# Kernel optimization log

Hardware: AMD Instinct MI355X
Metric: run time of the kernel (lower is better)

Reference implementation:

```python
import jax, jax.numpy as jnp
import numpy as np
from jax import lax

B, N, D_PTS = 8, 4096, 6
N_POINTS, N_SAMPLES, RADIUS = 1024, 32, 0.2
MLPS = [64, 64, 128]
BN_EPS = 1e-3  # keras BatchNormalization default epsilon


def safe_norm(diff, axis):
    # euclidean norm with a backward-safe sqrt (same forward values)
    sq = jnp.sum(diff * diff, axis=axis)
    pos = sq > 0
    return jnp.where(pos, jnp.sqrt(jnp.where(pos, sq, 1.0)), 0.0)


def setup_inputs() -> dict:
    key = jax.random.key(0)
    ks = jax.random.split(key, 2)
    xyz = jax.random.normal(ks[0], (B, N, 3), jnp.float32)
    points = jax.random.normal(ks[1], (B, N, D_PTS), jnp.float32)
    inp = {"xyz": xyz, "points": points}
    c_in = 3 + D_PTS
    for i, c_out in enumerate(MLPS):
        kw = jax.random.fold_in(key, 100 + i)
        inp[f"w{i}"] = jax.random.normal(kw, (c_in, c_out), jnp.float32) * (1.0 / np.sqrt(c_in))
        inp[f"b{i}"] = jnp.zeros((c_out,), jnp.float32)
        inp[f"g{i}"] = jnp.ones((c_out,), jnp.float32)
        inp[f"be{i}"] = jnp.zeros((c_out,), jnp.float32)
        c_in = c_out
    return inp


def fps(xyz, n_points):
    # farthest point sampling; original seeds with a random index, we use 0 deterministically
    b, n, _ = xyz.shape
    init_idx = jnp.zeros((b,), jnp.int32)
    mask0 = jnp.ones((b, n), xyz.dtype)
    def step(carry, _):
        mask, last = carry
        added = jnp.take_along_axis(xyz, last[:, None, None], axis=1)  # [B,1,D]
        dist = safe_norm(xyz - added, 2) * mask                        # [B,N]
        nxt = jnp.argmax(dist, axis=1).astype(jnp.int32)
        new_mask = jnp.minimum(dist * mask * 1e11, mask)
        return (new_mask, nxt), nxt
    _, ids = lax.scan(step, (mask0, init_idx), None, length=n_points - 1)
    return jnp.concatenate([init_idx[:, None], ids.T], axis=1)  # [B, n_points]


def gather_points(x, idx):
    # x: [B,N,C]; idx: [B,...] -> [B,...,C]
    b = x.shape[0]
    flat = idx.reshape(b, -1)
    out = jnp.take_along_axis(x, flat[..., None], axis=1)
    return out.reshape(idx.shape + (x.shape[-1],))


def query_ball(radius, n_samples, xyz, cent_xyz):
    # faithful to source: compares norm to radius**2 (source quirk), full argsort then slice
    diff = xyz[:, None, :, :] - cent_xyz[:, :, None, :]   # [B,n,N,3]
    dist = safe_norm(diff, 3)                              # [B,n,N]
    dist = jnp.minimum(dist, radius * radius)
    return jnp.argsort(dist, axis=2)[:, :, :n_samples]     # [B,n,n_samples]


def mlp_layer(h, w, b, g, be):
    # pointwise Dense + BatchNormalization (batch stats, axis=-1) + relu
    h = jnp.einsum('bnsc,cd->bnsd', h, w) + b
    mean = jnp.mean(h, axis=(0, 1, 2), keepdims=True)
    var = jnp.var(h, axis=(0, 1, 2), keepdims=True)
    h = g * (h - mean) * lax.rsqrt(var + BN_EPS) + be
    return jax.nn.relu(h)


def forward(xyz, points, params):
    cent_idx = fps(xyz, N_POINTS)                 # [B, n_points]
    cent_xyz = gather_points(xyz, cent_idx)       # [B, n_points, 3]
    group_idx = query_ball(RADIUS, N_SAMPLES, xyz, cent_xyz)  # [B, n_points, n_samples]
    group_xyz = gather_points(xyz, group_idx)     # [B, n_points, n_samples, 3]
    group_pts = gather_points(points, group_idx)  # [B, n_points, n_samples, D]
    h = jnp.concatenate([group_xyz, group_pts], axis=-1)
    for (w, b, g, be) in params:
        h = mlp_layer(h, w, b, g, be)
    return cent_xyz, jnp.max(h, axis=2)           # [B,n_points,3], [B,n_points,128]


def reference(xyz, points, w0, b0, g0, be0, w1, b1, g1, be1, w2, b2, g2, be2):
    params = [(w0, b0, g0, be0), (w1, b1, g1, be1), (w2, b2, g2, be2)]
    return forward(xyz, points, params)
```

## Files before the change

kernel.cpp:

```cpp
#include <hip/hip_runtime.h>

#define NPTS  4096
#define NB    8
#define NC    1024
#define NSAMP 32
#define DP    6
#define C0    9
#define C3    128
#define ROWS_TOT 262144

#define OFF_SS   (32ull<<10)
#define OFF_Y0   (16ull<<20)
#define OFF_Y1   (96ull<<20)
#define OFF_PSUM (168ull<<20)
#define OFF_PSQ  (172ull<<20)
#define OFF_GMX  (176ull<<20)
#define OFF_GMN  (180ull<<20)

typedef unsigned long long ull;

__device__ __forceinline__ float sqdist_noc(float x, float y, float z,
                                            float cx, float cy, float cz) {
  #pragma clang fp contract(off)
  float dx = x - cx, dy = y - cy, dz = z - cz;
  return dx * dx + dy * dy + dz * dz;
}

template <int CTRL, int RM>
__device__ __forceinline__ float dpp_mov_f(float x) {
  int xi = __float_as_int(x);
  int r = __builtin_amdgcn_update_dpp(xi, xi, CTRL, RM, 0xf, false);
  return __int_as_float(r);
}

__device__ __forceinline__ float wave64_fmax(float x) {
  x = fmaxf(x, dpp_mov_f<0x111, 0xf>(x));
  x = fmaxf(x, dpp_mov_f<0x112, 0xf>(x));
  x = fmaxf(x, dpp_mov_f<0x114, 0xf>(x));
  x = fmaxf(x, dpp_mov_f<0x118, 0xf>(x));
  x = fmaxf(x, dpp_mov_f<0x142, 0xa>(x));
  x = fmaxf(x, dpp_mov_f<0x143, 0xc>(x));
  return x;
}

__global__ __launch_bounds__(256)
void fps_kernel(const float* __restrict__ xyz, float* __restrict__ cent) {
  const int b = blockIdx.x;
  const int t = threadIdx.x;
  const float* X = xyz + (size_t)b * NPTS * 3;
  float* OC = cent + (size_t)b * NC * 3;

  __shared__ float4 sxyz[NPTS];
  __shared__ float4 wkc[2][4];
  __shared__ alignas(16) int wki[2][4];
  __shared__ int sidx[NC];

  for (int p = t; p < NPTS; p += 256)
    sxyz[p] = make_float4(X[p * 3 + 0], X[p * 3 + 1], X[p * 3 + 2], 0.f);
  __syncthreads();

  float px[16], py[16], pz[16], h[16];
  #pragma unroll
  for (int i = 0; i < 16; i++) {
    float4 v = sxyz[t * 16 + i];
    px[i] = v.x; py[i] = v.y; pz[i] = v.z;
    h[i] = fmaf(v.x, v.x, fmaf(v.y, v.y, v.z * v.z));
  }

  const int wv = t >> 6;
  float4 c;

  auto step_body = [&](int pw_) {
    const float c2x = c.x + c.x, c2y = c.y + c.y, c2z = c.z + c.z;
    float key[16]; int idx[16];
    #pragma unroll
    for (int i = 0; i < 16; i++) {
      key[i] = fmaf(pz[i], -c2z, fmaf(py[i], -c2y, fmaf(px[i], -c2x, h[i])));
      idx[i] = i;
    }
    #pragma unroll
    for (int s = 1; s < 16; s <<= 1) {
      #pragma unroll
      for (int i = 0; i < 16; i += 2 * s) {
        bool tk = key[i + s] > key[i];
        key[i] = tk ? key[i + s] : key[i];
        idx[i] = tk ? idx[i + s] : idx[i];
      }
    }
    const float mx = key[0];
    const int mj = idx[0];
    float4 cand = sxyz[(t << 4) + mj];
    float wm = wave64_fmax(mx);
    float smax = __int_as_float(__builtin_amdgcn_readlane(__float_as_int(wm), 63));
    if (mx == smax) {
      wkc[pw_][wv] = make_float4(cand.x, cand.y, cand.z, smax);
      wki[pw_][wv] = (t << 4) + mj;
    }
  };

  auto fold = [&](int pr_) -> int {
    float4 q0 = wkc[pr_][0], q1 = wkc[pr_][1];
    float4 q2 = wkc[pr_][2], q3 = wkc[pr_][3];
    const int4 ii = *(const int4*)&wki[pr_][0];
    bool g1 = q1.w > q0.w; float4 ca = g1 ? q1 : q0; int ia = g1 ? ii.y : ii.x;
    bool g3 = q3.w > q2.w; float4 cb = g3 ? q3 : q2; int ib = g3 ? ii.w : ii.z;
    bool gb = cb.w > ca.w; c = gb ? cb : ca; return gb ? ib : ia;
  };

  if (t == 0) { sidx[0] = 0; h[0] = -__builtin_inff(); }
  c = sxyz[0];
  step_body(1);
  __syncthreads();

  for (int k = 2; k < NC; k++) {
    const int pr = (k - 1) & 1, pw = k & 1;
    int gidx = fold(pr);
    if (t == 0) sidx[k - 1] = gidx;
    if ((gidx >> 4) == t) {
      int m = gidx & 15;
      #pragma unroll
      for (int i = 0; i < 16; i++)
        if (i == m) h[i] = -__builtin_inff();
    }
    step_body(pw);
    __syncthreads();
  }
  {
    int gidx = fold(1023 & 1);
    if (t == 0) sidx[NC - 1] = gidx;
  }
  __syncthreads();
  for (int i = t; i < NC; i += 256) {
    float4 cc = sxyz[sidx[i]];
    OC[i * 3 + 0] = cc.x;
    OC[i * 3 + 1] = cc.y;
    OC[i * 3 + 2] = cc.z;
  }
}

#define BCAP 256
__global__ __launch_bounds__(256)
void ball_dense0_kernel(const float* __restrict__ xyz, const float* __restrict__ pts,
                        const float* __restrict__ cent,
                        const float* __restrict__ W0, const float* __restrict__ b0,
                        float* __restrict__ y0,
                        float* __restrict__ psum, float* __restrict__ psq) {
  const int blk = blockIdx.x;
  const int b = blk >> 10;
  const int t = threadIdx.x;
  const float* X = xyz + (size_t)b * NPTS * 3;
  const float* P = pts + (size_t)b * NPTS * DP;
  const float cx = cent[(size_t)blk * 3 + 0];
  const float cy = cent[(size_t)blk * 3 + 1];
  const float cz = cent[(size_t)blk * 3 + 2];

  __shared__ int scount;
  __shared__ ull skeys[BCAP];
  __shared__ ull ssorted[BCAP];
  __shared__ int sel[NSAMP];
  __shared__ float xs0[NSAMP * C0];
  __shared__ float w0s[C0 * 64];
  __shared__ float b0s[64];
  __shared__ float red[2][NSAMP][64];
  if (t == 0) scount = 0;
  for (int e = t; e < C0 * 64; e += 256) w0s[e] = W0[e];
  if (t < 64) b0s[t] = b0[t];
  __syncthreads();

  #pragma unroll
  for (int i = 0; i < 16; i++) {
    int j = t * 16 + i;
    float sq = sqdist_noc(X[j * 3 + 0], X[j * 3 + 1], X[j * 3 + 2], cx, cy, cz);
    if (sq < 0.0017f) {
      float d = (sq > 0.f) ? sqrtf(sq) : 0.f;
      if (d < 0.04f) {
        int pos = atomicAdd(&scount, 1);
        if (pos < BCAP)
          skeys[pos] = ((ull)(unsigned)__float_as_int(d) << 12) | (unsigned)j;
      }
    }
  }
  __syncthreads();
  const int M = min(scount, BCAP);

  if (t < M) {
    ull my = skeys[t];
    int r = 0;
    for (int j2 = 0; j2 < M; j2++) r += (skeys[j2] < my);
    ssorted[r] = my;
  }
  __syncthreads();

  if (t < NSAMP) {
    int v;
    if (t < M) {
      v = (int)(ssorted[t] & 0xFFFull);
    } else {
      int s = t - M;
      int idx = s;
      for (int it = 0; it < 40; it++) {
        int c = 0;
        for (int j2 = 0; j2 < M; j2++) c += ((int)(skeys[j2] & 0xFFFull) <= idx);
        int nidx = s + c;
        if (nidx == idx) break;
        idx = nidx;
      }
      v = idx;
    }
    sel[t] = v;
  }
  __syncthreads();

  for (int e = t; e < NSAMP * C0; e += 256) {
    int k = e / C0;
    int cc = e - k * C0;
    int j = sel[k];
    xs0[e] = (cc < 3) ? X[j * 3 + cc] : P[j * DP + (cc - 3)];
  }
  __syncthreads();

  const int row = t >> 3, c8 = (t & 7) * 8;
  float a[8];
  #pragma unroll
  for (int j = 0; j < 8; j++) a[j] = b0s[c8 + j];
  #pragma unroll
  for (int k = 0; k < C0; k++) {
    float xv = xs0[row * C0 + k];
    #pragma unroll
    for (int j = 0; j < 8; j++) a[j] = fmaf(xv, w0s[k * 64 + c8 + j], a[j]);
  }
  float* Y = y0 + ((size_t)blk * NSAMP + row) * 64 + c8;
  *(float4*)(Y + 0) = make_float4(a[0], a[1], a[2], a[3]);
  *(float4*)(Y + 4) = make_float4(a[4], a[5], a[6], a[7]);
  #pragma unroll
  for (int j = 0; j < 8; j++) red[0][row][c8 + j] = a[j];
  #pragma unroll
  for (int j = 0; j < 8; j++) red[1][row][c8 + j] = a[j] * a[j];
  __syncthreads();
  if (t < 64) {
    float S = 0.f, Q = 0.f;
    #pragma unroll
    for (int g = 0; g < NSAMP; g++) { S += red[0][g][t]; Q += red[1][g][t]; }
    psum[(size_t)t * 8192 + blk] = S;
    psq [(size_t)t * 8192 + blk] = Q;
  }
}

template <int RPB, int COUT, int CGN, int NBLKS, bool MM>
__global__ __launch_bounds__(256)
void dense_mid_kernel(const float* __restrict__ yin, const float* __restrict__ ssin,
                      const float* __restrict__ W, const float* __restrict__ bias,
                      float* __restrict__ yout,
                      float* __restrict__ psum, float* __restrict__ psq,
                      float* __restrict__ gmax, float* __restrict__ gmin) {
  constexpr int NG = 256 / CGN;
  __shared__ float xs[RPB * 68];
  __shared__ float ws[64 * COUT];
  __shared__ float scs[64], shs[64];
  __shared__ float red[2][NG][COUT];
  __shared__ float redm[MM ? 2 : 1][MM ? NG : 1][MM ? COUT : 1];
  const int blk = blockIdx.x, t = threadIdx.x;
  if (t < 64) { scs[t] = ssin[t]; shs[t] = ssin[128 + t]; }
  __syncthreads();
  const size_t rbase = (size_t)blk * RPB;
  for (int e = t; e < RPB * 64; e += 256) {
    int c = e & 63;
    float v = yin[rbase * 64 + e];
    xs[(e >> 6) * 68 + c] = fmaxf(fmaf(v, scs[c], shs[c]), 0.f);
  }
  for (int e = t; e < 64 * COUT; e += 256) ws[e] = W[e];
  __syncthreads();
  const int rg = t / CGN, cg = t % CGN;
  float acc[4][4];
  float4 bv = *(const float4*)(bias + cg * 4);
  #pragma unroll
  for (int r = 0; r < 4; r++) { acc[r][0] = bv.x; acc[r][1] = bv.y; acc[r][2] = bv.z; acc[r][3] = bv.w; }
  for (int k0 = 0; k0 < 64; k0 += 4) {
    float4 xv[4];
    #pragma unroll
    for (int r = 0; r < 4; r++)
      xv[r] = *(const float4*)(xs + (rg * 4 + r) * 68 + k0);
    #pragma unroll
    for (int kk = 0; kk < 4; kk++) {
      float4 wv = *(const float4*)(ws + (k0 + kk) * COUT + cg * 4);
      #pragma unroll
      for (int r = 0; r < 4; r++) {
        float x = (&xv[r].x)[kk];
        acc[r][0] = fmaf(x, wv.x, acc[r][0]);
        acc[r][1] = fmaf(x, wv.y, acc[r][1]);
        acc[r][2] = fmaf(x, wv.z, acc[r][2]);
        acc[r][3] = fmaf(x, wv.w, acc[r][3]);
      }
    }
  }
  if constexpr (!MM) {
    #pragma unroll
    for (int r = 0; r < 4; r++)
      *(float4*)(yout + (rbase + rg * 4 + r) * COUT + cg * 4) =
          make_float4(acc[r][0], acc[r][1], acc[r][2], acc[r][3]);
  }
  #pragma unroll
  for (int c4 = 0; c4 < 4; c4++) {
    float s = 0.f, q = 0.f;
    #pragma unroll
    for (int r = 0; r < 4; r++) { float v = acc[r][c4]; s += v; q = fmaf(v, v, q); }
    red[0][rg][cg * 4 + c4] = s;
    red[1][rg][cg * 4 + c4] = q;
    if constexpr (MM) {
      float mx = acc[0][c4], mn = acc[0][c4];
      #pragma unroll
      for (int r = 1; r < 4; r++) { mx = fmaxf(mx, acc[r][c4]); mn = fminf(mn, acc[r][c4]); }
      redm[0][rg][cg * 4 + c4] = mx;
      redm[1][rg][cg * 4 + c4] = mn;
    }
  }
  __syncthreads();
  if (t < COUT) {
    float S = 0.f, Q = 0.f;
    #pragma unroll
    for (int g = 0; g < NG; g++) { S += red[0][g][t]; Q += red[1][g][t]; }
    psum[(size_t)t * NBLKS + blk] = S;
    psq [(size_t)t * NBLKS + blk] = Q;
    if constexpr (MM) {
      float mx = redm[0][0][t], mn = redm[1][0][t];
      #pragma unroll
      for (int g = 1; g < NG; g++) { mx = fmaxf(mx, redm[0][g][t]); mn = fminf(mn, redm[1][g][t]); }
      gmax[(size_t)blk * COUT + t] = mx;
      gmin[(size_t)blk * COUT + t] = mn;
    }
  }
}

template <int NBLK>
__global__ __launch_bounds__(256)
void stats_final_kernel(const float* __restrict__ psum, const float* __restrict__ psq,
                        const float* __restrict__ g, const float* __restrict__ be,
                        float* __restrict__ ss_out) {
  const int c = blockIdx.x, t = threadIdx.x;
  float S = 0.f, Q = 0.f;
  for (int i = t; i < NBLK; i += 256) {
    S += psum[(size_t)c * NBLK + i];
    Q += psq [(size_t)c * NBLK + i];
  }
  __shared__ float sS[256], sQ[256];
  sS[t] = S; sQ[t] = Q;
  __syncthreads();
  #pragma unroll
  for (int off = 128; off; off >>= 1) {
    if (t < off) { sS[t] += sS[t + off]; sQ[t] += sQ[t + off]; }
    __syncthreads();
  }
  if (t == 0) {
    const float inv = 1.0f / 262144.0f;
    float mean = sS[0] * inv;
    float var = sQ[0] * inv - mean * mean;
    float scale = g[c] / sqrtf(var + 1e-3f);
    ss_out[c] = scale;
    ss_out[128 + c] = be[c] - mean * scale;
  }
}

__global__ __launch_bounds__(128)
void pool_final_kernel(const float* __restrict__ gmax, const float* __restrict__ gmin,
                       const float* __restrict__ ss2, float* __restrict__ out1) {
  const int blk = blockIdx.x, c = threadIdx.x;
  const float sc = ss2[c], sh = ss2[128 + c];
  float v = (sc >= 0.f) ? gmax[(size_t)blk * C3 + c] : gmin[(size_t)blk * C3 + c];
  out1[(size_t)blk * C3 + c] = fmaxf(fmaf(v, sc, sh), 0.f);
}

extern "C" void kernel_launch(void* const* d_in, const int* in_sizes, int n_in,
                              void* d_out, int out_size, void* d_ws, size_t ws_size,
                              hipStream_t stream) {
  const float* xyz = (const float*)d_in[0];
  const float* pts = (const float*)d_in[1];
  const float* w0 = (const float*)d_in[2];
  const float* b0 = (const float*)d_in[3];
  const float* g0 = (const float*)d_in[4];
  const float* be0 = (const float*)d_in[5];
  const float* w1 = (const float*)d_in[6];
  const float* b1 = (const float*)d_in[7];
  const float* g1 = (const float*)d_in[8];
  const float* be1 = (const float*)d_in[9];
  const float* w2 = (const float*)d_in[10];
  const float* b2 = (const float*)d_in[11];
  const float* g2 = (const float*)d_in[12];
  const float* be2 = (const float*)d_in[13];

  float* out = (float*)d_out;
  float* cent = out;
  float* out1 = out + (size_t)NB * NC * 3;

  char* ws = (char*)d_ws;
  float* ssA  = (float*)(ws + OFF_SS);
  float* y0   = (float*)(ws + OFF_Y0);
  float* y1   = (float*)(ws + OFF_Y1);
  float* psum = (float*)(ws + OFF_PSUM);
  float* psq  = (float*)(ws + OFF_PSQ);
  float* gmx  = (float*)(ws + OFF_GMX);
  float* gmn  = (float*)(ws + OFF_GMN);

  fps_kernel<<<dim3(NB), dim3(256), 0, stream>>>(xyz, cent);

  ball_dense0_kernel<<<dim3(NB * NC), dim3(256), 0, stream>>>(
      xyz, pts, cent, w0, b0, y0, psum, psq);
  stats_final_kernel<8192><<<dim3(64), dim3(256), 0, stream>>>(psum, psq, g0, be0, ssA + 0 * 256);

  dense_mid_kernel<64, 64, 16, 4096, false><<<dim3(ROWS_TOT / 64), dim3(256), 0, stream>>>(
      y0, ssA + 0 * 256, w1, b1, y1, psum, psq, nullptr, nullptr);
  stats_final_kernel<4096><<<dim3(64), dim3(256), 0, stream>>>(psum, psq, g1, be1, ssA + 1 * 256);

  dense_mid_kernel<32, 128, 32, 8192, true><<<dim3(ROWS_TOT / 32), dim3(256), 0, stream>>>(
      y1, ssA + 1 * 256, w2, b2, nullptr, psum, psq, gmx, gmn);
  stats_final_kernel<8192><<<dim3(128), dim3(256), 0, stream>>>(psum, psq, g2, be2, ssA + 2 * 256);

  pool_final_kernel<<<dim3(NB * NC), dim3(128), 0, stream>>>(gmx, gmn, ssA + 2 * 256, out1);

  (void)in_sizes; (void)n_in; (void)out_size; (void)ws_size;
}
```

Measured before the change: 880.8 us.

## Use one-row-per-thread dense kernels with uniform weight reads and transposed reductions

The shared-memory tiled register-blocked dense kernels for layers 1 and 2 are replaced by kernels where each thread computes a full output row. Weights are read straight from global memory with wave-uniform indices, so they can become scalar loads, and the input tile staging through LDS is removed. Per-channel sum, sum of squares and per-centroid max/min are computed by transposing accumulators through padded LDS. Holding 64 accumulators plus 64 inputs per thread raises register pressure and may lower occupancy. The non-coalesced per-thread row loads are another risk.

```diff
diff --git a/kernel.cpp b/kernel.cpp
--- a/kernel.cpp
+++ b/kernel.cpp
@@ -246,88 +246,131 @@
   }
 }
 
-template <int RPB, int COUT, int CGN, int NBLKS, bool MM>
 __global__ __launch_bounds__(256)
-void dense_mid_kernel(const float* __restrict__ yin, const float* __restrict__ ssin,
-                      const float* __restrict__ W, const float* __restrict__ bias,
-                      float* __restrict__ yout,
-                      float* __restrict__ psum, float* __restrict__ psq,
-                      float* __restrict__ gmax, float* __restrict__ gmin) {
-  constexpr int NG = 256 / CGN;
-  __shared__ float xs[RPB * 68];
-  __shared__ float ws[64 * COUT];
-  __shared__ float scs[64], shs[64];
-  __shared__ float red[2][NG][COUT];
-  __shared__ float redm[MM ? 2 : 1][MM ? NG : 1][MM ? COUT : 1];
-  const int blk = blockIdx.x, t = threadIdx.x;
-  if (t < 64) { scs[t] = ssin[t]; shs[t] = ssin[128 + t]; }
-  __syncthreads();
-  const size_t rbase = (size_t)blk * RPB;
-  for (int e = t; e < RPB * 64; e += 256) {
-    int c = e & 63;
-    float v = yin[rbase * 64 + e];
-    xs[(e >> 6) * 68 + c] = fmaxf(fmaf(v, scs[c], shs[c]), 0.f);
-  }
-  for (int e = t; e < 64 * COUT; e += 256) ws[e] = W[e];
-  __syncthreads();
-  const int rg = t / CGN, cg = t % CGN;
-  float acc[4][4];
-  float4 bv = *(const float4*)(bias + cg * 4);
-  #pragma unroll
-  for (int r = 0; r < 4; r++) { acc[r][0] = bv.x; acc[r][1] = bv.y; acc[r][2] = bv.z; acc[r][3] = bv.w; }
+void dense_lane1_kernel(const float* __restrict__ y0, const float* __restrict__ ss0,
+                        const float* __restrict__ W1, const float* __restrict__ b1,
+                        float* __restrict__ y1,
+                        float* __restrict__ psum, float* __restrict__ psq) {
+  __shared__ float tr[4][64][33];
+  __shared__ float wred[2][4][64];
+  const int t = threadIdx.x, wid = t >> 6, lane = t & 63;
+  const size_t row = (size_t)blockIdx.x * 256 + (size_t)(wid * 64 + lane);
+  float acc[64];
+  #pragma unroll
+  for (int c = 0; c < 64; c++) acc[c] = b1[c];
+  const float* Xr = y0 + row * 64;
+  #pragma unroll 1
   for (int k0 = 0; k0 < 64; k0 += 4) {
-    float4 xv[4];
-    #pragma unroll
-    for (int r = 0; r < 4; r++)
-      xv[r] = *(const float4*)(xs + (rg * 4 + r) * 68 + k0);
+    float4 xv = *(const float4*)(Xr + k0);
     #pragma unroll
     for (int kk = 0; kk < 4; kk++) {
-      float4 wv = *(const float4*)(ws + (k0 + kk) * COUT + cg * 4);
+      const int k = k0 + kk;
+      float x = fmaxf(fmaf((&xv.x)[kk], ss0[k], ss0[128 + k]), 0.f);
+      const float* Wk = W1 + k * 64;
       #pragma unroll
-      for (int r = 0; r < 4; r++) {
-        float x = (&xv[r].x)[kk];
-        acc[r][0] = fmaf(x, wv.x, acc[r][0]);
-        acc[r][1] = fmaf(x, wv.y, acc[r][1]);
-        acc[r][2] = fmaf(x, wv.z, acc[r][2]);
-        acc[r][3] = fmaf(x, wv.w, acc[r][3]);
-      }
-    }
-  }
-  if constexpr (!MM) {
-    #pragma unroll
-    for (int r = 0; r < 4; r++)
-      *(float4*)(yout + (rbase + rg * 4 + r) * COUT + cg * 4) =
-          make_float4(acc[r][0], acc[r][1], acc[r][2], acc[r][3]);
-  }
-  #pragma unroll
-  for (int c4 = 0; c4 < 4; c4++) {
-    float s = 0.f, q = 0.f;
-    #pragma unroll
-    for (int r = 0; r < 4; r++) { float v = acc[r][c4]; s += v; q = fmaf(v, v, q); }
-    red[0][rg][cg * 4 + c4] = s;
-    red[1][rg][cg * 4 + c4] = q;
-    if constexpr (MM) {
-      float mx = acc[0][c4], mn = acc[0][c4];
+      for (int c = 0; c < 64; c++) acc[c] = fmaf(x, Wk[c], acc[c]);
+    }
+  }
+  float* Yr = y1 + row * 64;
+  #pragma unroll
+  for (int c0 = 0; c0 < 64; c0 += 4)
+    *(float4*)(Yr + c0) = make_float4(acc[c0], acc[c0 + 1], acc[c0 + 2], acc[c0 + 3]);
+  const int c = lane & 31;
+  const bool isQ = lane >= 32;
+  #pragma unroll
+  for (int chunk = 0; chunk < 2; chunk++) {
+    __syncthreads();
+    #pragma unroll
+    for (int j = 0; j < 32; j++) tr[wid][lane][j] = acc[chunk * 32 + j];
+    __syncthreads();
+    float A = 0.f;
+    for (int r = 0; r < 64; r++) {
+      float v = tr[wid][r][c];
+      A = fmaf(v, isQ ? v : 1.0f, A);
+    }
+    wred[isQ ? 1 : 0][wid][chunk * 32 + c] = A;
+  }
+  __syncthreads();
+  if (t < 64) {
+    float S = 0.f, Q = 0.f;
+    #pragma unroll
+    for (int w = 0; w < 4; w++) { S += wred[0][w][t]; Q += wred[1][w][t]; }
+    psum[(size_t)t * 1024 + blockIdx.x] = S;
+    psq [(size_t)t * 1024 + blockIdx.x] = Q;
+  }
+}
+
+__global__ __launch_bounds__(256)
+void dense_lane2_kernel(const float* __restrict__ y1, const float* __restrict__ ss1,
+                        const float* __restrict__ W2, const float* __restrict__ b2,
+                        float* __restrict__ psum, float* __restrict__ psq,
+                        float* __restrict__ gmax, float* __restrict__ gmin) {
+  __shared__ float tr[4][64][33];
+  __shared__ float wred[2][4][128];
+  const int t = threadIdx.x, wid = t >> 6, lane = t & 63;
+  const size_t row = (size_t)blockIdx.x * 256 + (size_t)(wid * 64 + lane);
+  const int centA = blockIdx.x * 8 + wid * 2;
+  const int centB = centA + 1;
+
+  float x[64];
+  const float* Xr = y1 + row * 64;
+  #pragma unroll
+  for (int k0 = 0; k0 < 64; k0 += 4) {
+    float4 xv = *(const float4*)(Xr + k0);
+    #pragma unroll
+    for (int kk = 0; kk < 4; kk++)
+      x[k0 + kk] = fmaxf(fmaf((&xv.x)[kk], ss1[k0 + kk], ss1[128 + k0 + kk]), 0.f);
+  }
+
+  const int c = lane & 31;
+  const bool isQ = lane >= 32;
+  #pragma unroll 1
+  for (int half = 0; half < 2; half++) {
+    float acc[64];
+    #pragma unroll
+    for (int cc = 0; cc < 64; cc++) acc[cc] = b2[half * 64 + cc];
+    #pragma unroll 1
+    for (int k = 0; k < 64; k++) {
+      const float* Wk = W2 + k * C3 + half * 64;
+      const float xk = x[k];
       #pragma unroll
-      for (int r = 1; r < 4; r++) { mx = fmaxf(mx, acc[r][c4]); mn = fminf(mn, acc[r][c4]); }
-      redm[0][rg][cg * 4 + c4] = mx;
-      redm[1][rg][cg * 4 + c4] = mn;
-    }
-  }
-  __syncthreads();
-  if (t < COUT) {
+      for (int cc = 0; cc < 64; cc++) acc[cc] = fmaf(xk, Wk[cc], acc[cc]);
+    }
+    #pragma unroll
+    for (int chunk = 0; chunk < 2; chunk++) {
+      __syncthreads();
+      #pragma unroll
+      for (int j = 0; j < 32; j++) tr[wid][lane][j] = acc[chunk * 32 + j];
+      __syncthreads();
+      const int ch = half * 64 + chunk * 32 + c;
+      float A = 0.f, m1 = -__builtin_inff(), m2 = -__builtin_inff();
+      for (int r = 0; r < 32; r++) {
+        float v = tr[wid][r][c];
+        A = fmaf(v, isQ ? v : 1.0f, A);
+        m1 = fmaxf(m1, isQ ? -v : v);
+      }
+      for (int r = 32; r < 64; r++) {
+        float v = tr[wid][r][c];
+        A = fmaf(v, isQ ? v : 1.0f, A);
+        m2 = fmaxf(m2, isQ ? -v : v);
+      }
+      wred[isQ ? 1 : 0][wid][ch] = A;
+      if (!isQ) {
+        gmax[(size_t)centA * C3 + ch] = m1;
+        gmax[(size_t)centB * C3 + ch] = m2;
+      } else {
+        gmin[(size_t)centA * C3 + ch] = -m1;
+        gmin[(size_t)centB * C3 + ch] = -m2;
+      }
+    }
+  }
+  __syncthreads();
+  if (t < C3) {
     float S = 0.f, Q = 0.f;
     #pragma unroll
-    for (int g = 0; g < NG; g++) { S += red[0][g][t]; Q += red[1][g][t]; }
-    psum[(size_t)t * NBLKS + blk] = S;
-    psq [(size_t)t * NBLKS + blk] = Q;
-    if constexpr (MM) {
-      float mx = redm[0][0][t], mn = redm[1][0][t];
-      #pragma unroll
-      for (int g = 1; g < NG; g++) { mx = fmaxf(mx, redm[0][g][t]); mn = fminf(mn, redm[1][g][t]); }
-      gmax[(size_t)blk * COUT + t] = mx;
-      gmin[(size_t)blk * COUT + t] = mn;
-    }
+    for (int w = 0; w < 4; w++) { S += wred[0][w][t]; Q += wred[1][w][t]; }
+    psum[(size_t)t * 1024 + blockIdx.x] = S;
+    psq [(size_t)t * 1024 + blockIdx.x] = Q;
   }
 }
 
@@ -406,13 +449,13 @@
       xyz, pts, cent, w0, b0, y0, psum, psq);
   stats_final_kernel<8192><<<dim3(64), dim3(256), 0, stream>>>(psum, psq, g0, be0, ssA + 0 * 256);
 
-  dense_mid_kernel<64, 64, 16, 4096, false><<<dim3(ROWS_TOT / 64), dim3(256), 0, stream>>>(
-      y0, ssA + 0 * 256, w1, b1, y1, psum, psq, nullptr, nullptr);
-  stats_final_kernel<4096><<<dim3(64), dim3(256), 0, stream>>>(psum, psq, g1, be1, ssA + 1 * 256);
-
-  dense_mid_kernel<32, 128, 32, 8192, true><<<dim3(ROWS_TOT / 32), dim3(256), 0, stream>>>(
-      y1, ssA + 1 * 256, w2, b2, nullptr, psum, psq, gmx, gmn);
-  stats_final_kernel<8192><<<dim3(128), dim3(256), 0, stream>>>(psum, psq, g2, be2, ssA + 2 * 256);
+  dense_lane1_kernel<<<dim3(ROWS_TOT / 256), dim3(256), 0, stream>>>(
+      y0, ssA + 0 * 256, w1, b1, y1, psum, psq);
+  stats_final_kernel<1024><<<dim3(64), dim3(256), 0, stream>>>(psum, psq, g1, be1, ssA + 1 * 256);
+
+  dense_lane2_kernel<<<dim3(ROWS_TOT / 256), dim3(256), 0, stream>>>(
+      y1, ssA + 1 * 256, w2, b2, psum, psq, gmx, gmn);
+  stats_final_kernel<1024><<<dim3(128), dim3(256), 0, stream>>>(psum, psq, g2, be2, ssA + 2 * 256);
 
   pool_final_kernel<<<dim3(NB * NC), dim3(128), 0, stream>>>(gmx, gmn, ssA + 2 * 256, out1);
 
```

Result: no change. 874.2 us (-0.8%).
